# Kernel tuning notes

Hardware: AMD Instinct MI355X
Metric: run time of the kernel (lower is better)

## Reference

```python
import jax, jax.numpy as jnp
import numpy as np

# TT-linear: in_features=1024 -> out_features=4096
IN_DIMS = (8, 8, 4, 4)      # m1..m4, prod = 1024
OUT_DIMS = (8, 8, 8, 8)     # n1..n4, prod = 4096
RANKS = (1, 16, 16, 16, 1)  # r0..r4
IN_FEATURES = 1024
OUT_FEATURES = 4096
BATCH, SEQ = 4, 1024


def _init_core(key, shape):
    # uniform(-1,1)/sqrt(fan_in-ish), matching the original's uniform-style init scale
    fan = shape[0] * shape[1]
    return (2.0 * jax.random.uniform(key, shape, dtype=jnp.float32) - 1.0) / np.sqrt(fan).astype(np.float32)


def setup_inputs() -> dict:
    key = jax.random.key(0)
    ks = jax.random.split(key, 6)
    x = jax.random.normal(ks[0], (BATCH, SEQ, IN_FEATURES), dtype=jnp.float32)
    core0 = _init_core(ks[1], (1, 8, 8, 16))    # [r0, m1, n1, r1]
    core1 = _init_core(ks[2], (16, 8, 8, 16))   # [r1, m2, n2, r2]
    core2 = _init_core(ks[3], (16, 4, 8, 16))   # [r2, m3, n3, r3]
    core3 = _init_core(ks[4], (16, 4, 8, 1))    # [r3, m4, n4, r4]
    bias = (2.0 * jax.random.uniform(ks[5], (OUT_FEATURES,), dtype=jnp.float32) - 1.0) / np.sqrt(OUT_FEATURES).astype(np.float32)
    return {"x": x, "core0": core0, "core1": core1, "core2": core2, "core3": core3, "bias": bias}


def reference(x, core0, core1, core2, core3, bias):
    lead = x.shape[:-1]
    # split the feature axis into TT input factors: [T, m1, m2, m3, m4]
    t = x.reshape((-1,) + IN_DIMS)
    c0 = core0[0]        # [m1, n1, r1]   (boundary rank r0 = 1 squeezed)
    c3 = core3[..., 0]   # [r3, m4, n4]   (boundary rank r4 = 1 squeezed)
    # sequential TT core chain: absorb one m_k, emit one n_k per step
    t = jnp.einsum('tijkl,ixp->tjklxp', t, c0)      # [T, m2,m3,m4, n1, r1]
    t = jnp.einsum('tjklxp,pjyq->tklxyq', t, core1)  # [T, m3,m4, n1,n2, r2]
    t = jnp.einsum('tklxyq,qkzr->tlxyzr', t, core2)  # [T, m4, n1,n2,n3, r3]
    t = jnp.einsum('tlxyzr,rlw->txyzw', t, c3)       # [T, n1,n2,n3,n4]
    y = t.reshape(lead + (OUT_FEATURES,)) + bias
    return y
```

## Files before the change

### kernel.cpp

```cpp
#include <hip/hip_runtime.h>
#include <hip/hip_bf16.h>
#include <cstdint>


typedef __bf16 bf16x8 __attribute__((ext_vector_type(8)));
typedef float f32x4 __attribute__((ext_vector_type(4)));

__device__ __forceinline__ void g2lds16(const void* g, void* l) {
    __builtin_amdgcn_global_load_lds(
        (const __attribute__((address_space(1))) void*)g,
        (__attribute__((address_space(3))) void*)l,
        16, 0, 0);
}

__global__ __launch_bounds__(256) void prep(
    const float* __restrict__ x, __bf16* __restrict__ xb,
    const float* __restrict__ c0, const float* __restrict__ c1,
    const float* __restrict__ c2, const float* __restrict__ c3,
    __bf16* __restrict__ wt) {
    const int b = blockIdx.x;
    const int t = threadIdx.x;
    if (b < 2048) {
        const int i = (b * 256 + t) * 8;
        float4 a0 = *(const float4*)(x + i);
        float4 a1 = *(const float4*)(x + i + 4);
        bf16x8 o;
        o[0] = (__bf16)a0.x; o[1] = (__bf16)a0.y; o[2] = (__bf16)a0.z; o[3] = (__bf16)a0.w;
        o[4] = (__bf16)a1.x; o[5] = (__bf16)a1.y; o[6] = (__bf16)a1.z; o[7] = (__bf16)a1.w;
        *(bf16x8*)(xb + i) = o;
        return;
    }
    __shared__ float t12[4][16];
    __shared__ float t123[4][512];
    __shared__ float c3s[512];
    #pragma unroll
    for (int i = t; i < 512; i += 256) c3s[i] = c3[i];
    const int s = t >> 6;
    const int lane = t & 63;
    const int g = (b - 2048) * 4 + s;
    const int m1 = g >> 9, n1 = (g >> 6) & 7, m2 = (g >> 3) & 7, n2 = g & 7;
    __syncthreads();
    if (lane < 16) {
        const int r2 = lane;
        float sum = 0.f;
        #pragma unroll
        for (int r1 = 0; r1 < 16; ++r1)
            sum += c0[(m1 * 8 + n1) * 16 + r1] * c1[((r1 * 8 + m2) * 8 + n2) * 16 + r2];
        t12[s][r2] = sum;
    }
    __syncthreads();
    #pragma unroll
    for (int idx = lane; idx < 512; idx += 64) {
        const int m3 = idx >> 7, n3 = (idx >> 4) & 7, r3 = idx & 15;
        float sum = 0.f;
        #pragma unroll
        for (int r2 = 0; r2 < 16; ++r2)
            sum += t12[s][r2] * c2[((r2 * 4 + m3) * 8 + n3) * 16 + r3];
        t123[s][(m3 * 8 + n3) * 16 + r3] = sum;
    }
    __syncthreads();
    const int n3 = lane >> 3, n4 = lane & 7;
    const int n = ((n1 * 8 + n2) * 8 + n3) * 8 + n4;
    const int kbase = (m1 * 8 + m2) * 16;
    float v[16];
    #pragma unroll
    for (int e = 0; e < 16; ++e) v[e] = 0.f;
    #pragma unroll
    for (int m3 = 0; m3 < 4; ++m3) {
        #pragma unroll
        for (int r3 = 0; r3 < 16; ++r3) {
            const float tv = t123[s][(m3 * 8 + n3) * 16 + r3];
            #pragma unroll
            for (int m4 = 0; m4 < 4; ++m4)
                v[m3 * 4 + m4] += tv * c3s[(r3 * 4 + m4) * 8 + n4];
        }
    }
    bf16x8 lo, hi;
    #pragma unroll
    for (int e = 0; e < 8; ++e) { lo[e] = (__bf16)v[e]; hi[e] = (__bf16)v[8 + e]; }
    *(bf16x8*)(wt + (size_t)n * 1024 + kbase)     = lo;
    *(bf16x8*)(wt + (size_t)n * 1024 + kbase + 8) = hi;
}

__global__ __launch_bounds__(256) void tt_gemm(
    const __bf16* __restrict__ A, const __bf16* __restrict__ B,
    const float* __restrict__ bias, float* __restrict__ C) {
    constexpr int K = 1024, N = 4096;
    __shared__ __bf16 sA[128 * 64];
    __shared__ __bf16 sB[128 * 64];
    const int t = threadIdx.x;
    const int lane = t & 63;
    const int wave = t >> 6;
    const int wm = (wave >> 1) * 64;
    const int wn = (wave & 1) * 64;
    const int xcd = blockIdx.x & 7;
    const int lid = blockIdx.x >> 3;
    const int bm = (lid & 31) * 128;
    const int bn = (xcd * 4 + (lid >> 5)) * 128;
    const int l15 = lane & 15, lh = lane >> 4;
    const int swz = l15 & 7;

    f32x4 acc[4][4] = {};

    for (int k0 = 0; k0 < K; k0 += 64) {
        __syncthreads();
        #pragma unroll
        for (int i = 0; i < 4; ++i) {
            const int c = t + i * 256;
            const int r = c >> 3;
            const int gc = (c & 7) ^ (r & 7);
            g2lds16(A + (size_t)(bm + r) * K + k0 + gc * 8, (char*)sA + (size_t)c * 16);
            g2lds16(B + (size_t)(bn + r) * K + k0 + gc * 8, (char*)sB + (size_t)c * 16);
        }
        asm volatile("s_waitcnt vmcnt(0)" ::: "memory");
        __syncthreads();
        #pragma unroll
        for (int kk = 0; kk < 2; ++kk) {
            const int coff = ((kk * 4 + lh) ^ swz) * 16;
            bf16x8 af[4], bfr[4];
            #pragma unroll
            for (int mi = 0; mi < 4; ++mi)
                af[mi] = *(const bf16x8*)((const char*)sA + (size_t)(wm + mi * 16 + l15) * 128 + coff);
            #pragma unroll
            for (int ni = 0; ni < 4; ++ni)
                bfr[ni] = *(const bf16x8*)((const char*)sB + (size_t)(wn + ni * 16 + l15) * 128 + coff);
            #pragma unroll
            for (int mi = 0; mi < 4; ++mi)
                #pragma unroll
                for (int ni = 0; ni < 4; ++ni)
                    acc[mi][ni] = __builtin_amdgcn_mfma_f32_16x16x32_bf16(
                        af[mi], bfr[ni], acc[mi][ni], 0, 0, 0);
        }
    }

    #pragma unroll
    for (int ni = 0; ni < 4; ++ni) {
        const int col = bn + wn + ni * 16 + l15;
        const float bv = bias[col];
        #pragma unroll
        for (int mi = 0; mi < 4; ++mi) {
            const int row0 = bm + wm + mi * 16 + lh * 4;
            const f32x4 v = acc[mi][ni];
            #pragma unroll
            for (int r = 0; r < 4; ++r)
                C[(size_t)(row0 + r) * N + col] = v[r] + bv;
        }
    }
}

extern "C" void kernel_launch(void* const* d_in, const int* in_sizes, int n_in,
                              void* d_out, int out_size, void* d_ws, size_t ws_size,
                              hipStream_t stream) {
    const float* x    = (const float*)d_in[0];
    const float* c0   = (const float*)d_in[1];
    const float* c1   = (const float*)d_in[2];
    const float* c2   = (const float*)d_in[3];
    const float* c3   = (const float*)d_in[4];
    const float* bias = (const float*)d_in[5];
    float* out = (float*)d_out;

    __bf16* xb = (__bf16*)d_ws;
    __bf16* wt = xb + (size_t)4096 * 1024;

    prep<<<3072, 256, 0, stream>>>(x, xb, c0, c1, c2, c3, wt);
    tt_gemm<<<1024, 256, 0, stream>>>(xb, wt, bias, out);
}
```

Before: 142.3 us.

## Rework GEMM into 256x256 tiles with 4-stage async LDS pipeline

Replaces the 128x128-tile, single-buffered GEMM with 256x256 tiles on 512-thread blocks, K-step 32, and a 4-deep ring of LDS buffers filled by async global-to-LDS loads issued three stages ahead. Loads for A and B are interleaved between two half-tile MFMA phases, with s_setprio around the MFMA blocks, so memory latency overlaps with compute instead of stalling at every k-step. The larger tile raises data reuse per block. In exchange it uses more LDS and registers (launch bounds 512,2) and leaves only 256 blocks, which may underfill the GPU's compute units.

```diff
diff --git a/kernel.cpp b/kernel.cpp
--- a/kernel.cpp
+++ b/kernel.cpp
@@ -82,55 +82,121 @@
     *(bf16x8*)(wt + (size_t)n * 1024 + kbase + 8) = hi;
 }
 
-__global__ __launch_bounds__(256) void tt_gemm(
+
+#define BAR() asm volatile("s_barrier" ::: "memory")
+#define VMCNT(n) asm volatile("s_waitcnt vmcnt(" #n ")" ::: "memory")
+
+__global__ __launch_bounds__(512, 2) void tt_gemm(
     const __bf16* __restrict__ A, const __bf16* __restrict__ B,
     const float* __restrict__ bias, float* __restrict__ C) {
     constexpr int K = 1024, N = 4096;
-    __shared__ __bf16 sA[128 * 64];
-    __shared__ __bf16 sB[128 * 64];
+    constexpr int NT = K / 32;
+    __shared__ __bf16 sA[4][256 * 32];
+    __shared__ __bf16 sB[4][256 * 32];
     const int t = threadIdx.x;
     const int lane = t & 63;
     const int wave = t >> 6;
-    const int wm = (wave >> 1) * 64;
-    const int wn = (wave & 1) * 64;
+    const int wm = (wave >> 2) * 128;
+    const int wn = (wave & 3) * 64;
+    const int l15 = lane & 15, lh = lane >> 4;
+    const int coff = (lh ^ ((l15 >> 1) & 3)) * 16;
+
     const int xcd = blockIdx.x & 7;
     const int lid = blockIdx.x >> 3;
-    const int bm = (lid & 31) * 128;
-    const int bn = (xcd * 4 + (lid >> 5)) * 128;
-    const int l15 = lane & 15, lh = lane >> 4;
-    const int swz = l15 & 7;
-
-    f32x4 acc[4][4] = {};
-
-    for (int k0 = 0; k0 < K; k0 += 64) {
-        __syncthreads();
-        #pragma unroll
-        for (int i = 0; i < 4; ++i) {
-            const int c = t + i * 256;
-            const int r = c >> 3;
-            const int gc = (c & 7) ^ (r & 7);
-            g2lds16(A + (size_t)(bm + r) * K + k0 + gc * 8, (char*)sA + (size_t)c * 16);
-            g2lds16(B + (size_t)(bn + r) * K + k0 + gc * 8, (char*)sB + (size_t)c * 16);
-        }
-        asm volatile("s_waitcnt vmcnt(0)" ::: "memory");
-        __syncthreads();
-        #pragma unroll
-        for (int kk = 0; kk < 2; ++kk) {
-            const int coff = ((kk * 4 + lh) ^ swz) * 16;
-            bf16x8 af[4], bfr[4];
-            #pragma unroll
-            for (int mi = 0; mi < 4; ++mi)
-                af[mi] = *(const bf16x8*)((const char*)sA + (size_t)(wm + mi * 16 + l15) * 128 + coff);
-            #pragma unroll
-            for (int ni = 0; ni < 4; ++ni)
-                bfr[ni] = *(const bf16x8*)((const char*)sB + (size_t)(wn + ni * 16 + l15) * 128 + coff);
-            #pragma unroll
-            for (int mi = 0; mi < 4; ++mi)
-                #pragma unroll
-                for (int ni = 0; ni < 4; ++ni)
-                    acc[mi][ni] = __builtin_amdgcn_mfma_f32_16x16x32_bf16(
-                        af[mi], bfr[ni], acc[mi][ni], 0, 0, 0);
-        }
+    const int bm = ((xcd >> 2) * 8 + (lid & 7)) * 256;
+    const int bn = ((xcd & 3) * 4 + (lid >> 3)) * 256;
+
+    const int c0i = t, c1i = t + 512;
+    const int r0 = c0i >> 2, r1 = c1i >> 2;
+    const int lc0 = (c0i & 3) ^ ((r0 >> 1) & 3);
+    const int lc1 = (c1i & 3) ^ ((r1 >> 1) & 3);
+    const __bf16* a0p = A + (size_t)(bm + r0) * K + lc0 * 8;
+    const __bf16* a1p = A + (size_t)(bm + r1) * K + lc1 * 8;
+    const __bf16* b0p = B + (size_t)(bn + r0) * K + lc0 * 8;
+    const __bf16* b1p = B + (size_t)(bn + r1) * K + lc1 * 8;
+
+#define STAGE_A(kt) do { \
+    g2lds16(a0p + (kt) * 32, (char*)sA[(kt) & 3] + c0i * 16); \
+    g2lds16(a1p + (kt) * 32, (char*)sA[(kt) & 3] + c1i * 16); } while (0)
+#define STAGE_B(kt) do { \
+    g2lds16(b0p + (kt) * 32, (char*)sB[(kt) & 3] + c0i * 16); \
+    g2lds16(b1p + (kt) * 32, (char*)sB[(kt) & 3] + c1i * 16); } while (0)
+
+    f32x4 acc[8][4] = {};
+
+    STAGE_A(0); STAGE_B(0);
+    STAGE_A(1); STAGE_B(1);
+    STAGE_A(2); STAGE_B(2);
+    VMCNT(8);
+    BAR();
+
+    #pragma unroll 1
+    for (int kt = 0; kt < NT - 3; ++kt) {
+        const char* la = (const char*)sA[kt & 3];
+        const char* lb = (const char*)sB[kt & 3];
+        bf16x8 af[4], bfr[4];
+        #pragma unroll
+        for (int mi = 0; mi < 4; ++mi)
+            af[mi] = *(const bf16x8*)(la + (wm + mi * 16 + l15) * 64 + coff);
+        #pragma unroll
+        for (int ni = 0; ni < 4; ++ni)
+            bfr[ni] = *(const bf16x8*)(lb + (wn + ni * 16 + l15) * 64 + coff);
+        STAGE_A(kt + 3);
+        BAR();
+        __builtin_amdgcn_s_setprio(1);
+        #pragma unroll
+        for (int mi = 0; mi < 4; ++mi)
+            #pragma unroll
+            for (int ni = 0; ni < 4; ++ni)
+                acc[mi][ni] = __builtin_amdgcn_mfma_f32_16x16x32_bf16(
+                    af[mi], bfr[ni], acc[mi][ni], 0, 0, 0);
+        __builtin_amdgcn_s_setprio(0);
+        BAR();
+        #pragma unroll
+        for (int mi = 0; mi < 4; ++mi)
+            af[mi] = *(const bf16x8*)(la + (wm + 64 + mi * 16 + l15) * 64 + coff);
+        STAGE_B(kt + 3);
+        VMCNT(8);
+        BAR();
+        __builtin_amdgcn_s_setprio(1);
+        #pragma unroll
+        for (int mi = 0; mi < 4; ++mi)
+            #pragma unroll
+            for (int ni = 0; ni < 4; ++ni)
+                acc[4 + mi][ni] = __builtin_amdgcn_mfma_f32_16x16x32_bf16(
+                    af[mi], bfr[ni], acc[4 + mi][ni], 0, 0, 0);
+        __builtin_amdgcn_s_setprio(0);
+        BAR();
+    }
+
+    VMCNT(0);
+    BAR();
+    #pragma unroll
+    for (int kt = NT - 3; kt < NT; ++kt) {
+        const char* la = (const char*)sA[kt & 3];
+        const char* lb = (const char*)sB[kt & 3];
+        bf16x8 af[4], bfr[4];
+        #pragma unroll
+        for (int ni = 0; ni < 4; ++ni)
+            bfr[ni] = *(const bf16x8*)(lb + (wn + ni * 16 + l15) * 64 + coff);
+        #pragma unroll
+        for (int mi = 0; mi < 4; ++mi)
+            af[mi] = *(const bf16x8*)(la + (wm + mi * 16 + l15) * 64 + coff);
+        #pragma unroll
+        for (int mi = 0; mi < 4; ++mi)
+            #pragma unroll
+            for (int ni = 0; ni < 4; ++ni)
+                acc[mi][ni] = __builtin_amdgcn_mfma_f32_16x16x32_bf16(
+                    af[mi], bfr[ni], acc[mi][ni], 0, 0, 0);
+        #pragma unroll
+        for (int mi = 0; mi < 4; ++mi)
+            af[mi] = *(const bf16x8*)(la + (wm + 64 + mi * 16 + l15) * 64 + coff);
+        #pragma unroll
+        for (int mi = 0; mi < 4; ++mi)
+            #pragma unroll
+            for (int ni = 0; ni < 4; ++ni)
+                acc[4 + mi][ni] = __builtin_amdgcn_mfma_f32_16x16x32_bf16(
+                    af[mi], bfr[ni], acc[4 + mi][ni], 0, 0, 0);
     }
 
     #pragma unroll
@@ -138,7 +204,7 @@
         const int col = bn + wn + ni * 16 + l15;
         const float bv = bias[col];
         #pragma unroll
-        for (int mi = 0; mi < 4; ++mi) {
+        for (int mi = 0; mi < 8; ++mi) {
             const int row0 = bm + wm + mi * 16 + lh * 4;
             const f32x4 v = acc[mi][ni];
             #pragma unroll
@@ -146,6 +212,8 @@
                 C[(size_t)(row0 + r) * N + col] = v[r] + bv;
         }
     }
+#undef STAGE_A
+#undef STAGE_B
 }
 
 extern "C" void kernel_launch(void* const* d_in, const int* in_sizes, int n_in,
@@ -163,5 +231,5 @@
     __bf16* wt = xb + (size_t)4096 * 1024;
 
     prep<<<3072, 256, 0, stream>>>(x, xb, c0, c1, c2, c3, wt);
-    tt_gemm<<<1024, 256, 0, stream>>>(xb, wt, bias, out);
-}
+    tt_gemm<<<256, 512, 0, stream>>>(xb, wt, bias, out);
+}
```

Result: slower. 147.6 us (+3.7%).

## Rewrite GEMM with 256x256 tiles, 8 waves and double-buffered LDS pipeline

Applied to the files above, without the earlier changes.

The bf16 GEMM now uses 256x256 block tiles with 512 threads, where each wave computes a 128x64 sub-tile. Global-to-LDS loads go into a double buffer split into K halves, and staging of the next tiles is interleaved with MFMA phases using explicit barriers, s_setprio and partial vmcnt waits. The aim is to hide global load latency and raise arithmetic intensity per LDS byte. In exchange it uses more LDS and registers and launches only 256 blocks, which risks occupancy and tail imbalance across CUs.

```diff
diff --git a/kernel.cpp b/kernel.cpp
--- a/kernel.cpp
+++ b/kernel.cpp
@@ -82,70 +82,122 @@
     *(bf16x8*)(wt + (size_t)n * 1024 + kbase + 8) = hi;
 }
 
-__global__ __launch_bounds__(256) void tt_gemm(
+
+#define SCHED() __builtin_amdgcn_sched_barrier(0)
+#define BAR()  do { SCHED(); __builtin_amdgcn_s_barrier(); SCHED(); } while (0)
+#define WAITVM(n) do { SCHED(); asm volatile("s_waitcnt vmcnt(" #n ")"); SCHED(); } while (0)
+
+__global__ __launch_bounds__(512, 2) void tt_gemm(
     const __bf16* __restrict__ A, const __bf16* __restrict__ B,
     const float* __restrict__ bias, float* __restrict__ C) {
     constexpr int K = 1024, N = 4096;
-    __shared__ __bf16 sA[128 * 64];
-    __shared__ __bf16 sB[128 * 64];
+    constexpr int NKT = 16;
+    __shared__ __bf16 sA[2][2][256 * 32];
+    __shared__ __bf16 sB[2][2][256 * 32];
     const int t = threadIdx.x;
     const int lane = t & 63;
     const int wave = t >> 6;
-    const int wm = (wave >> 1) * 64;
-    const int wn = (wave & 1) * 64;
+    const int wm = (wave >> 2) * 128;
+    const int wn = (wave & 3) * 64;
+    const int l15 = lane & 15, lh = lane >> 4;
+    const int cOff = ((lh ^ (l15 & 3)) << 4);
+
     const int xcd = blockIdx.x & 7;
     const int lid = blockIdx.x >> 3;
-    const int bm = (lid & 31) * 128;
-    const int bn = (xcd * 4 + (lid >> 5)) * 128;
-    const int l15 = lane & 15, lh = lane >> 4;
-    const int swz = l15 & 7;
-
-    f32x4 acc[4][4] = {};
-
-    for (int k0 = 0; k0 < K; k0 += 64) {
-        __syncthreads();
-        #pragma unroll
-        for (int i = 0; i < 4; ++i) {
-            const int c = t + i * 256;
-            const int r = c >> 3;
-            const int gc = (c & 7) ^ (r & 7);
-            g2lds16(A + (size_t)(bm + r) * K + k0 + gc * 8, (char*)sA + (size_t)c * 16);
-            g2lds16(B + (size_t)(bn + r) * K + k0 + gc * 8, (char*)sB + (size_t)c * 16);
-        }
-        asm volatile("s_waitcnt vmcnt(0)" ::: "memory");
-        __syncthreads();
-        #pragma unroll
-        for (int kk = 0; kk < 2; ++kk) {
-            const int coff = ((kk * 4 + lh) ^ swz) * 16;
-            bf16x8 af[4], bfr[4];
-            #pragma unroll
-            for (int mi = 0; mi < 4; ++mi)
-                af[mi] = *(const bf16x8*)((const char*)sA + (size_t)(wm + mi * 16 + l15) * 128 + coff);
+    const int bm = ((xcd >> 2) * 8 + (lid & 7)) * 256;
+    const int bn = ((xcd & 3) * 4 + (lid >> 3)) * 256;
+
+    const int c0i = t, c1i = t + 512;
+    const int r0 = c0i >> 2, r1 = c1i >> 2;
+    const int lc0 = (c0i & 3) ^ (r0 & 3);
+    const int lc1 = (c1i & 3) ^ (r1 & 3);
+    const __bf16* a0p = A + (size_t)(bm + r0) * K + lc0 * 8;
+    const __bf16* a1p = A + (size_t)(bm + r1) * K + lc1 * 8;
+    const __bf16* b0p = B + (size_t)(bn + r0) * K + lc0 * 8;
+    const __bf16* b1p = B + (size_t)(bn + r1) * K + lc1 * 8;
+
+#define ST_A(kt, ks) do { \
+    g2lds16(a0p + (size_t)(kt) * 64 + (ks) * 32, (char*)&sA[(kt) & 1][ks][0] + c0i * 16); \
+    g2lds16(a1p + (size_t)(kt) * 64 + (ks) * 32, (char*)&sA[(kt) & 1][ks][0] + c1i * 16); } while (0)
+#define ST_B(kt, ks) do { \
+    g2lds16(b0p + (size_t)(kt) * 64 + (ks) * 32, (char*)&sB[(kt) & 1][ks][0] + c0i * 16); \
+    g2lds16(b1p + (size_t)(kt) * 64 + (ks) * 32, (char*)&sB[(kt) & 1][ks][0] + c1i * 16); } while (0)
+#define LDA(dst, fi, ks) dst = *(const bf16x8*)((const char*)&sA[slot][ks][0] + (wm + (fi) * 16 + l15) * 64 + cOff)
+#define LDB(dst, ni, ks) dst = *(const bf16x8*)((const char*)&sB[slot][ks][0] + (wn + (ni) * 16 + l15) * 64 + cOff)
+#define MFMA16(base, afr) do { \
+    __builtin_amdgcn_s_setprio(1); \
+    _Pragma("unroll") \
+    for (int mi = 0; mi < 4; ++mi) \
+        _Pragma("unroll") \
+        for (int ni = 0; ni < 4; ++ni) \
+            acc[(base) + mi][ni] = __builtin_amdgcn_mfma_f32_16x16x32_bf16( \
+                afr[mi], bb[ni], acc[(base) + mi][ni], 0, 0, 0); \
+    __builtin_amdgcn_s_setprio(0); } while (0)
+
+    f32x4 acc[8][4] = {};
+
+    ST_A(0, 0); ST_B(0, 0);
+    ST_A(0, 1); ST_B(0, 1);
+    ST_A(1, 0); ST_B(1, 0);
+    WAITVM(8);
+    BAR();
+
+    #pragma unroll 1
+    for (int kt = 0; kt < NKT; ++kt) {
+        const int slot = kt & 1;
+        bf16x8 aL[4], aH[4], bb[4];
+        #pragma unroll
+        for (int mi = 0; mi < 4; ++mi) LDA(aL[mi], mi, 0);
+        #pragma unroll
+        for (int ni = 0; ni < 4; ++ni) LDB(bb[ni], ni, 0);
+        if (kt < NKT - 1) ST_A(kt + 1, 1);
+        BAR();
+        MFMA16(0, aL);
+        BAR();
+        #pragma unroll
+        for (int mi = 0; mi < 4; ++mi) LDA(aH[mi], 4 + mi, 0);
+        if (kt < NKT - 1) ST_B(kt + 1, 1);
+        BAR();
+        MFMA16(4, aH);
+        if (kt < NKT - 1) { WAITVM(8); } else { WAITVM(0); }
+        BAR();
+        #pragma unroll
+        for (int mi = 0; mi < 4; ++mi) LDA(aL[mi], mi, 1);
+        #pragma unroll
+        for (int ni = 0; ni < 4; ++ni) LDB(bb[ni], ni, 1);
+        if (kt < NKT - 2) ST_A(kt + 2, 0);
+        BAR();
+        MFMA16(0, aL);
+        BAR();
+        #pragma unroll
+        for (int mi = 0; mi < 4; ++mi) LDA(aH[mi], 4 + mi, 1);
+        if (kt < NKT - 2) ST_B(kt + 2, 0);
+        BAR();
+        MFMA16(4, aH);
+        if (kt < NKT - 2)      { WAITVM(8); }
+        else if (kt == NKT - 2) { WAITVM(4); }
+        BAR();
+    }
+
+    float bv[4];
+    #pragma unroll
+    for (int ni = 0; ni < 4; ++ni) bv[ni] = bias[bn + wn + ni * 16 + l15];
+    #pragma unroll
+    for (int mi = 0; mi < 8; ++mi) {
+        #pragma unroll
+        for (int r = 0; r < 4; ++r) {
+            const int row = bm + wm + mi * 16 + lh * 4 + r;
+            float* crow = C + (size_t)row * N + bn + wn + l15;
             #pragma unroll
             for (int ni = 0; ni < 4; ++ni)
-                bfr[ni] = *(const bf16x8*)((const char*)sB + (size_t)(wn + ni * 16 + l15) * 128 + coff);
-            #pragma unroll
-            for (int mi = 0; mi < 4; ++mi)
-                #pragma unroll
-                for (int ni = 0; ni < 4; ++ni)
-                    acc[mi][ni] = __builtin_amdgcn_mfma_f32_16x16x32_bf16(
-                        af[mi], bfr[ni], acc[mi][ni], 0, 0, 0);
+                crow[ni * 16] = acc[mi][ni][r] + bv[ni];
         }
     }
-
-    #pragma unroll
-    for (int ni = 0; ni < 4; ++ni) {
-        const int col = bn + wn + ni * 16 + l15;
-        const float bv = bias[col];
-        #pragma unroll
-        for (int mi = 0; mi < 4; ++mi) {
-            const int row0 = bm + wm + mi * 16 + lh * 4;
-            const f32x4 v = acc[mi][ni];
-            #pragma unroll
-            for (int r = 0; r < 4; ++r)
-                C[(size_t)(row0 + r) * N + col] = v[r] + bv;
-        }
-    }
+#undef ST_A
+#undef ST_B
+#undef LDA
+#undef LDB
+#undef MFMA16
 }
 
 extern "C" void kernel_launch(void* const* d_in, const int* in_sizes, int n_in,
@@ -163,5 +215,5 @@
     __bf16* wt = xb + (size_t)4096 * 1024;
 
     prep<<<3072, 256, 0, stream>>>(x, xb, c0, c1, c2, c3, wt);
-    tt_gemm<<<1024, 256, 0, stream>>>(xb, wt, bias, out);
-}
+    tt_gemm<<<256, 512, 0, stream>>>(xb, wt, bias, out);
+}
```

Result: no change. 139.8 us (-1.7%).
